# Performance work log

Hardware: AMD Instinct MI355X
Metric: run time of the kernel (lower is better)

The kernel has to match this reference:

```python
import jax, jax.numpy as jnp
import numpy as np

N_NODES = 50000
N_EDGES = 800000
D_IN = 64
D_OUT = 64


def setup_inputs() -> dict:
    key = jax.random.key(0)
    k1, k2, k3 = jax.random.split(key, 3)
    features = jax.random.normal(k1, (N_NODES, D_IN), dtype=jnp.float32)
    W = jax.random.normal(k2, (D_IN, D_OUT), dtype=jnp.float32) * (1.0 / np.sqrt(D_IN))
    b = jnp.zeros((D_OUT,), dtype=jnp.float32)
    edge_index = jax.random.randint(k3, (2, N_EDGES), 0, N_NODES, dtype=jnp.int64)
    return {"features": features, "W": W, "b": b, "edge_index": edge_index}


def reference(features, W, b, edge_index):
    # PyG GCNConv: add self-loops, symmetric normalization D^{-1/2}(A+I)D^{-1/2},
    # then aggregate x[row] at col (source -> target), plus linear + bias.
    N = features.shape[0]
    loop = jnp.arange(N, dtype=edge_index.dtype)
    row = jnp.concatenate([edge_index[0], loop])  # source nodes
    col = jnp.concatenate([edge_index[1], loop])  # target nodes

    ones = jnp.ones(row.shape[0], dtype=features.dtype)
    deg = jax.ops.segment_sum(ones, col, num_segments=N)  # in-degree incl. self-loop
    dinv = jnp.where(deg > 0, jax.lax.rsqrt(deg), 0.0)
    norm = dinv[row] * dinv[col]  # [E+N]

    x = features @ W                          # [N, D_OUT], tiny GEMM
    msg = x[row] * norm[:, None]              # gather + scale  [E+N, D_OUT]
    out = jax.ops.segment_sum(msg, col, num_segments=N)  # scatter-add
    return out + b
```

## Files before the change

kernel.cpp:

```cpp
#include <hip/hip_runtime.h>
#include <hip/hip_fp16.h>

#define NN 50000
#define NE 800000
#define D  64
#define NBUK  256
#define NBLKS 500
#define CHUNK2 1600
#define HSTR  512
#define FS 68

typedef float __attribute__((ext_vector_type(4))) f32x4;

__device__ inline int block_exscan(int val, int tid) {
    __shared__ int wsum[4];
    int lane = tid & 63, w = tid >> 6;
    int v = val;
    #pragma unroll
    for (int d = 1; d < 64; d <<= 1) {
        int t = __shfl_up(v, d);
        if (lane >= d) v += t;
    }
    if (lane == 63) wsum[w] = v;
    __syncthreads();
    int base = 0;
    #pragma unroll
    for (int i = 0; i < 4; ++i) base += (i < w) ? wsum[i] : 0;
    __syncthreads();
    return base + v - val;
}

__global__ __launch_bounds__(256) void k_hist(const int* __restrict__ col,
                                              int* __restrict__ H) {
    __shared__ int h[NBUK];
    const int tid = threadIdx.x, blk = blockIdx.x;
    h[tid] = 0;
    __syncthreads();
    const uint4* col4 = reinterpret_cast<const uint4*>(col + blk * CHUNK2);
    for (int i = tid; i < CHUNK2 / 4; i += 256) {
        uint4 v = col4[i];
        atomicAdd(&h[v.x >> 8], 1);
        atomicAdd(&h[v.y >> 8], 1);
        atomicAdd(&h[v.z >> 8], 1);
        atomicAdd(&h[v.w >> 8], 1);
    }
    __syncthreads();
    H[tid * HSTR + blk] = h[tid];
}

__global__ __launch_bounds__(256) void k_scanA(int* __restrict__ H,
                                               int* __restrict__ bsum) {
    const int tid = threadIdx.x, bkt = blockIdx.x;
    int* Hb = H + bkt * HSTR;
    int v0 = 0, v1 = 0;
    if (tid < 250) { v0 = Hb[2 * tid]; v1 = Hb[2 * tid + 1]; }
    int sum = v0 + v1;
    int ex = block_exscan(sum, tid);
    if (tid < 250) { Hb[2 * tid] = ex; Hb[2 * tid + 1] = ex + v0; }
    if (tid == 255) bsum[bkt] = ex;
}

__global__ __launch_bounds__(256) void k_bucket(const int* __restrict__ row,
                                                const int* __restrict__ col,
                                                const int* __restrict__ H,
                                                const int* __restrict__ bsum,
                                                unsigned int* __restrict__ packed) {
    __shared__ int base_l[NBUK];
    __shared__ int rank[NBUK];
    const int tid = threadIdx.x, blk = blockIdx.x;
    int ex = block_exscan(bsum[tid], tid);
    base_l[tid] = ex + H[tid * HSTR + blk];
    rank[tid] = 0;
    __syncthreads();
    const uint4* col4 = reinterpret_cast<const uint4*>(col + blk * CHUNK2);
    const uint4* row4 = reinterpret_cast<const uint4*>(row + blk * CHUNK2);
    for (int i = tid; i < CHUNK2 / 4; i += 256) {
        uint4 c4 = col4[i];
        uint4 r4 = row4[i];
        #pragma unroll
        for (int e = 0; e < 4; ++e) {
            unsigned c = (e == 0) ? c4.x : (e == 1) ? c4.y : (e == 2) ? c4.z : c4.w;
            unsigned r = (e == 0) ? r4.x : (e == 1) ? r4.y : (e == 2) ? r4.z : r4.w;
            int bk = c >> 8;
            int rk = atomicAdd(&rank[bk], 1);
            packed[base_l[bk] + rk] = (r & 0xFFFF) | ((c & 0xFF) << 16);
        }
    }
}

__global__ __launch_bounds__(256) void k_csr(const unsigned int* __restrict__ packed,
                                             const int* __restrict__ bsum,
                                             int* __restrict__ off,
                                             int* __restrict__ cnt,
                                             unsigned short* __restrict__ csr) {
    __shared__ int exs[NBUK];
    __shared__ int ncnt[NBUK];
    __shared__ int nbase[NBUK];
    __shared__ int rk2[NBUK];
    const int tid = threadIdx.x, b = blockIdx.x;
    int ex = block_exscan(bsum[tid], tid);
    exs[tid] = ex;
    ncnt[tid] = 0;
    rk2[tid] = 0;
    __syncthreads();
    const int start = exs[b];
    const int size  = bsum[b];
    for (int i = tid; i < size; i += 256)
        atomicAdd(&ncnt[(packed[start + i] >> 16) & 0xFF], 1);
    __syncthreads();
    int v2  = ncnt[tid];
    int ex2 = block_exscan(v2, tid);
    const int node = b * NBUK + tid;
    off[node] = start + ex2;
    cnt[node] = v2;
    nbase[tid] = start + ex2;
    __syncthreads();
    for (int i = tid; i < size; i += 256) {
        unsigned u = packed[start + i];
        int ln = (u >> 16) & 0xFF;
        int rk = atomicAdd(&rk2[ln], 1);
        csr[nbase[ln] + rk] = (unsigned short)(u & 0xFFFF);
    }
}

__global__ __launch_bounds__(256) void k_gemm(const float* __restrict__ feat,
                                              const float* __restrict__ W,
                                              const int* __restrict__ cnt,
                                              __half* __restrict__ y) {
    __shared__ float feat_lds[64 * FS];
    __shared__ float W_lds[D * D];

    const int tid   = threadIdx.x;
    const int rbase = blockIdx.x * 64;

    {
        const float4* W4  = reinterpret_cast<const float4*>(W);
        float4*       Wl4 = reinterpret_cast<float4*>(W_lds);
        for (int i = tid; i < D * D / 4; i += 256) Wl4[i] = W4[i];
    }
    {
        const int k0 = (tid & 15) * 4;
        #pragma unroll
        for (int it = 0; it < 4; ++it) {
            int r  = it * 16 + (tid >> 4);
            int gr = rbase + r;
            float4 v = make_float4(0.f, 0.f, 0.f, 0.f);
            if (gr < NN) v = *reinterpret_cast<const float4*>(&feat[gr * D + k0]);
            *reinterpret_cast<float4*>(&feat_lds[r * FS + k0]) = v;
        }
    }
    __syncthreads();

    const int tx = tid & 15;
    const int ty = tid >> 4;

    float acc[4][4] = {};

    #pragma unroll 8
    for (int k = 0; k < D; ++k) {
        float4 w = *reinterpret_cast<const float4*>(&W_lds[k * D + tx * 4]);
        float f0 = feat_lds[(ty * 4 + 0) * FS + k];
        float f1 = feat_lds[(ty * 4 + 1) * FS + k];
        float f2 = feat_lds[(ty * 4 + 2) * FS + k];
        float f3 = feat_lds[(ty * 4 + 3) * FS + k];
        acc[0][0] = fmaf(f0, w.x, acc[0][0]); acc[0][1] = fmaf(f0, w.y, acc[0][1]);
        acc[0][2] = fmaf(f0, w.z, acc[0][2]); acc[0][3] = fmaf(f0, w.w, acc[0][3]);
        acc[1][0] = fmaf(f1, w.x, acc[1][0]); acc[1][1] = fmaf(f1, w.y, acc[1][1]);
        acc[1][2] = fmaf(f1, w.z, acc[1][2]); acc[1][3] = fmaf(f1, w.w, acc[1][3]);
        acc[2][0] = fmaf(f2, w.x, acc[2][0]); acc[2][1] = fmaf(f2, w.y, acc[2][1]);
        acc[2][2] = fmaf(f2, w.z, acc[2][2]); acc[2][3] = fmaf(f2, w.w, acc[2][3]);
        acc[3][0] = fmaf(f3, w.x, acc[3][0]); acc[3][1] = fmaf(f3, w.y, acc[3][1]);
        acc[3][2] = fmaf(f3, w.z, acc[3][2]); acc[3][3] = fmaf(f3, w.w, acc[3][3]);
    }

    #pragma unroll
    for (int i = 0; i < 4; ++i) {
        int gr = rbase + ty * 4 + i;
        if (gr < NN) {
            float s = rsqrtf((float)cnt[gr] + 1.0f);
            __half2 h0 = __floats2half2_rn(acc[i][0] * s, acc[i][1] * s);
            __half2 h1 = __floats2half2_rn(acc[i][2] * s, acc[i][3] * s);
            union { __half2 h[2]; uint2 u; } p;
            p.h[0] = h0; p.h[1] = h1;
            *reinterpret_cast<uint2*>(&y[gr * D + tx * 4]) = p.u;
        }
    }
}

__global__ __launch_bounds__(256, 8) void k_agg8(const unsigned short* __restrict__ csr,
                                                 const int* __restrict__ off,
                                                 const int* __restrict__ cnt,
                                                 const __half* __restrict__ y,
                                                 const float* __restrict__ b,
                                                 float* __restrict__ out) {
    const int lane = threadIdx.x & 63;
    const int g    = lane >> 3;
    const int l8   = lane & 7;
    const int wave = blockIdx.x * 4 + (threadIdx.x >> 6);
    const int c    = wave * 8 + g;
    const bool valid = (c < NN);

    const uint4* y16 = reinterpret_cast<const uint4*>(y);

    const int s = valid ? off[c] : 0;
    const int n = valid ? cnt[c] : 0;

    int pre0 = (l8      < n) ? (int)csr[s + l8     ] : 0;
    int pre1 = (l8 + 8  < n) ? (int)csr[s + l8 + 8 ] : 0;
    int pre2 = (l8 + 16 < n) ? (int)csr[s + l8 + 16] : 0;
    int pre3 = (l8 + 24 < n) ? (int)csr[s + l8 + 24] : 0;

    float acc[8] = {0.f, 0.f, 0.f, 0.f, 0.f, 0.f, 0.f, 0.f};

    auto addm = [&](uint4 u, float m) {
        const __half2* h = reinterpret_cast<const __half2*>(&u);
        float2 f0 = __half22float2(h[0]);
        float2 f1 = __half22float2(h[1]);
        float2 f2 = __half22float2(h[2]);
        float2 f3 = __half22float2(h[3]);
        acc[0] = fmaf(m, f0.x, acc[0]); acc[1] = fmaf(m, f0.y, acc[1]);
        acc[2] = fmaf(m, f1.x, acc[2]); acc[3] = fmaf(m, f1.y, acc[3]);
        acc[4] = fmaf(m, f2.x, acc[4]); acc[5] = fmaf(m, f2.y, acc[5]);
        acc[6] = fmaf(m, f3.x, acc[6]); acc[7] = fmaf(m, f3.y, acc[7]);
    };

    if (valid) addm(y16[c * 8 + l8], 1.0f);

    const int srcb = lane & 56;

    #pragma unroll
    for (int w = 0; w < 4; ++w) {
        if (w * 8 < n) {
            const int pw = (w == 0) ? pre0 : (w == 1) ? pre1
                         : (w == 2) ? pre2 : pre3;
            uint4 u[8];
            float msk[8];
            #pragma unroll
            for (int e = 0; e < 8; ++e) {
                int r = __shfl(pw, srcb + e);
                u[e] = y16[r * 8 + l8];
                msk[e] = (w * 8 + e < n) ? 1.0f : 0.0f;
            }
            #pragma unroll
            for (int e = 0; e < 8; ++e) addm(u[e], msk[e]);
        }
    }

    for (int i = 32; i < n; ++i) {
        int r = (int)csr[s + i];
        addm(y16[r * 8 + l8], 1.0f);
    }

    if (valid) {
        float sc = rsqrtf((float)n + 1.0f);
        const float4* b4 = reinterpret_cast<const float4*>(b);
        float4 bb0 = b4[l8 * 2], bb1 = b4[l8 * 2 + 1];
        f32x4 o0, o1;
        o0.x = acc[0] * sc + bb0.x;  o0.y = acc[1] * sc + bb0.y;
        o0.z = acc[2] * sc + bb0.z;  o0.w = acc[3] * sc + bb0.w;
        o1.x = acc[4] * sc + bb1.x;  o1.y = acc[5] * sc + bb1.y;
        o1.z = acc[6] * sc + bb1.z;  o1.w = acc[7] * sc + bb1.w;
        f32x4* out4 = reinterpret_cast<f32x4*>(out);
        __builtin_nontemporal_store(o0, &out4[c * 16 + l8 * 2]);
        __builtin_nontemporal_store(o1, &out4[c * 16 + l8 * 2 + 1]);
    }
}

extern "C" void kernel_launch(void* const* d_in, const int* in_sizes, int n_in,
                              void* d_out, int out_size, void* d_ws, size_t ws_size,
                              hipStream_t stream) {
    const float* feat = (const float*)d_in[0];
    const float* W    = (const float*)d_in[1];
    const float* b    = (const float*)d_in[2];
    const int*   ei   = (const int*)d_in[3];
    const int*   row  = ei;
    const int*   col  = ei + NE;

    float* out = (float*)d_out;

    int*            H      = (int*)d_ws;
    int*            bsum   = H + NBUK * HSTR;
    int*            cnt    = bsum + 1024;
    int*            off    = cnt + 65536;
    unsigned int*   packed = (unsigned int*)(off + 65536);
    unsigned short* csr    = (unsigned short*)(packed + NE);
    __half*         y      = (__half*)(csr + NE);

    k_hist  <<<NBLKS, 256, 0, stream>>>(col, H);
    k_scanA <<<NBUK,  256, 0, stream>>>(H, bsum);
    k_bucket<<<NBLKS, 256, 0, stream>>>(row, col, H, bsum, packed);
    k_csr   <<<NBUK,  256, 0, stream>>>(packed, bsum, off, cnt, csr);
    k_gemm  <<<(NN + 63) / 64, 256, 0, stream>>>(feat, W, cnt, y);
    k_agg8  <<<(NN + 31) / 32, 256, 0, stream>>>(csr, off, cnt, y, b, out);
}
```

Before: 57.62 us.

## Fuse histogram with GEMM, move source-degree scaling into aggregation, stage CSR in LDS

The column histogram and the feature GEMM now run in one launch, split by block index, so the GEMM no longer waits for the CSR build and one launch is removed. The GEMM output is left unscaled. A per-node dinv array is produced in k_csr and applied per edge during aggregation, which adds a dinv[r] gather for every edge. k_csr also stages each bucket's packed edges and the local CSR in LDS before writing them out coalesced, and keeps a global-memory fallback for buckets that exceed the capacity.

```diff
diff --git a/kernel.cpp b/kernel.cpp
--- a/kernel.cpp
+++ b/kernel.cpp
@@ -9,6 +9,8 @@
 #define CHUNK2 1600
 #define HSTR  512
 #define FS 68
+#define GEMMB 782
+#define CAP 8192
 
 typedef float __attribute__((ext_vector_type(4))) f32x4;
 
@@ -30,108 +32,35 @@
     return base + v - val;
 }
 
-__global__ __launch_bounds__(256) void k_hist(const int* __restrict__ col,
-                                              int* __restrict__ H) {
-    __shared__ int h[NBUK];
-    const int tid = threadIdx.x, blk = blockIdx.x;
-    h[tid] = 0;
-    __syncthreads();
-    const uint4* col4 = reinterpret_cast<const uint4*>(col + blk * CHUNK2);
-    for (int i = tid; i < CHUNK2 / 4; i += 256) {
-        uint4 v = col4[i];
-        atomicAdd(&h[v.x >> 8], 1);
-        atomicAdd(&h[v.y >> 8], 1);
-        atomicAdd(&h[v.z >> 8], 1);
-        atomicAdd(&h[v.w >> 8], 1);
-    }
-    __syncthreads();
-    H[tid * HSTR + blk] = h[tid];
-}
-
-__global__ __launch_bounds__(256) void k_scanA(int* __restrict__ H,
-                                               int* __restrict__ bsum) {
-    const int tid = threadIdx.x, bkt = blockIdx.x;
-    int* Hb = H + bkt * HSTR;
-    int v0 = 0, v1 = 0;
-    if (tid < 250) { v0 = Hb[2 * tid]; v1 = Hb[2 * tid + 1]; }
-    int sum = v0 + v1;
-    int ex = block_exscan(sum, tid);
-    if (tid < 250) { Hb[2 * tid] = ex; Hb[2 * tid + 1] = ex + v0; }
-    if (tid == 255) bsum[bkt] = ex;
-}
-
-__global__ __launch_bounds__(256) void k_bucket(const int* __restrict__ row,
-                                                const int* __restrict__ col,
-                                                const int* __restrict__ H,
-                                                const int* __restrict__ bsum,
-                                                unsigned int* __restrict__ packed) {
-    __shared__ int base_l[NBUK];
-    __shared__ int rank[NBUK];
-    const int tid = threadIdx.x, blk = blockIdx.x;
-    int ex = block_exscan(bsum[tid], tid);
-    base_l[tid] = ex + H[tid * HSTR + blk];
-    rank[tid] = 0;
-    __syncthreads();
-    const uint4* col4 = reinterpret_cast<const uint4*>(col + blk * CHUNK2);
-    const uint4* row4 = reinterpret_cast<const uint4*>(row + blk * CHUNK2);
-    for (int i = tid; i < CHUNK2 / 4; i += 256) {
-        uint4 c4 = col4[i];
-        uint4 r4 = row4[i];
-        #pragma unroll
-        for (int e = 0; e < 4; ++e) {
-            unsigned c = (e == 0) ? c4.x : (e == 1) ? c4.y : (e == 2) ? c4.z : c4.w;
-            unsigned r = (e == 0) ? r4.x : (e == 1) ? r4.y : (e == 2) ? r4.z : r4.w;
-            int bk = c >> 8;
-            int rk = atomicAdd(&rank[bk], 1);
-            packed[base_l[bk] + rk] = (r & 0xFFFF) | ((c & 0xFF) << 16);
-        }
-    }
-}
-
-__global__ __launch_bounds__(256) void k_csr(const unsigned int* __restrict__ packed,
-                                             const int* __restrict__ bsum,
-                                             int* __restrict__ off,
-                                             int* __restrict__ cnt,
-                                             unsigned short* __restrict__ csr) {
-    __shared__ int exs[NBUK];
-    __shared__ int ncnt[NBUK];
-    __shared__ int nbase[NBUK];
-    __shared__ int rk2[NBUK];
-    const int tid = threadIdx.x, b = blockIdx.x;
-    int ex = block_exscan(bsum[tid], tid);
-    exs[tid] = ex;
-    ncnt[tid] = 0;
-    rk2[tid] = 0;
-    __syncthreads();
-    const int start = exs[b];
-    const int size  = bsum[b];
-    for (int i = tid; i < size; i += 256)
-        atomicAdd(&ncnt[(packed[start + i] >> 16) & 0xFF], 1);
-    __syncthreads();
-    int v2  = ncnt[tid];
-    int ex2 = block_exscan(v2, tid);
-    const int node = b * NBUK + tid;
-    off[node] = start + ex2;
-    cnt[node] = v2;
-    nbase[tid] = start + ex2;
-    __syncthreads();
-    for (int i = tid; i < size; i += 256) {
-        unsigned u = packed[start + i];
-        int ln = (u >> 16) & 0xFF;
-        int rk = atomicAdd(&rk2[ln], 1);
-        csr[nbase[ln] + rk] = (unsigned short)(u & 0xFFFF);
-    }
-}
-
-__global__ __launch_bounds__(256) void k_gemm(const float* __restrict__ feat,
-                                              const float* __restrict__ W,
-                                              const int* __restrict__ cnt,
-                                              __half* __restrict__ y) {
-    __shared__ float feat_lds[64 * FS];
-    __shared__ float W_lds[D * D];
-
-    const int tid   = threadIdx.x;
-    const int rbase = blockIdx.x * 64;
+__global__ __launch_bounds__(256) void k_hist_gemm(const int* __restrict__ col,
+                                                   int* __restrict__ H,
+                                                   const float* __restrict__ feat,
+                                                   const float* __restrict__ W,
+                                                   __half* __restrict__ y) {
+    __shared__ float smem[64 * FS + D * D];
+    const int tid = threadIdx.x;
+
+    if (blockIdx.x < NBLKS) {
+        int* h = reinterpret_cast<int*>(smem);
+        const int blk = blockIdx.x;
+        h[tid] = 0;
+        __syncthreads();
+        const uint4* col4 = reinterpret_cast<const uint4*>(col + blk * CHUNK2);
+        for (int i = tid; i < CHUNK2 / 4; i += 256) {
+            uint4 v = col4[i];
+            atomicAdd(&h[v.x >> 8], 1);
+            atomicAdd(&h[v.y >> 8], 1);
+            atomicAdd(&h[v.z >> 8], 1);
+            atomicAdd(&h[v.w >> 8], 1);
+        }
+        __syncthreads();
+        H[tid * HSTR + blk] = h[tid];
+        return;
+    }
+
+    float* feat_lds = smem;
+    float* W_lds    = smem + 64 * FS;
+    const int rbase = (blockIdx.x - NBLKS) * 64;
 
     {
         const float4* W4  = reinterpret_cast<const float4*>(W);
@@ -177,9 +106,8 @@
     for (int i = 0; i < 4; ++i) {
         int gr = rbase + ty * 4 + i;
         if (gr < NN) {
-            float s = rsqrtf((float)cnt[gr] + 1.0f);
-            __half2 h0 = __floats2half2_rn(acc[i][0] * s, acc[i][1] * s);
-            __half2 h1 = __floats2half2_rn(acc[i][2] * s, acc[i][3] * s);
+            __half2 h0 = __floats2half2_rn(acc[i][0], acc[i][1]);
+            __half2 h1 = __floats2half2_rn(acc[i][2], acc[i][3]);
             union { __half2 h[2]; uint2 u; } p;
             p.h[0] = h0; p.h[1] = h1;
             *reinterpret_cast<uint2*>(&y[gr * D + tx * 4]) = p.u;
@@ -187,9 +115,116 @@
     }
 }
 
+__global__ __launch_bounds__(256) void k_scanA(int* __restrict__ H,
+                                               int* __restrict__ bsum) {
+    const int tid = threadIdx.x, bkt = blockIdx.x;
+    int* Hb = H + bkt * HSTR;
+    int v0 = 0, v1 = 0;
+    if (tid < 250) { v0 = Hb[2 * tid]; v1 = Hb[2 * tid + 1]; }
+    int sum = v0 + v1;
+    int ex = block_exscan(sum, tid);
+    if (tid < 250) { Hb[2 * tid] = ex; Hb[2 * tid + 1] = ex + v0; }
+    if (tid == 255) bsum[bkt] = ex;
+}
+
+__global__ __launch_bounds__(256) void k_bucket(const int* __restrict__ row,
+                                                const int* __restrict__ col,
+                                                const int* __restrict__ H,
+                                                const int* __restrict__ bsum,
+                                                unsigned int* __restrict__ packed) {
+    __shared__ int base_l[NBUK];
+    __shared__ int rank[NBUK];
+    const int tid = threadIdx.x, blk = blockIdx.x;
+    int ex = block_exscan(bsum[tid], tid);
+    base_l[tid] = ex + H[tid * HSTR + blk];
+    rank[tid] = 0;
+    __syncthreads();
+    const uint4* col4 = reinterpret_cast<const uint4*>(col + blk * CHUNK2);
+    const uint4* row4 = reinterpret_cast<const uint4*>(row + blk * CHUNK2);
+    for (int i = tid; i < CHUNK2 / 4; i += 256) {
+        uint4 c4 = col4[i];
+        uint4 r4 = row4[i];
+        #pragma unroll
+        for (int e = 0; e < 4; ++e) {
+            unsigned c = (e == 0) ? c4.x : (e == 1) ? c4.y : (e == 2) ? c4.z : c4.w;
+            unsigned r = (e == 0) ? r4.x : (e == 1) ? r4.y : (e == 2) ? r4.z : r4.w;
+            int bk = c >> 8;
+            int rk = atomicAdd(&rank[bk], 1);
+            packed[base_l[bk] + rk] = (r & 0xFFFF) | ((c & 0xFF) << 16);
+        }
+    }
+}
+
+__global__ __launch_bounds__(256) void k_csr(const unsigned int* __restrict__ packed,
+                                             const int* __restrict__ bsum,
+                                             int* __restrict__ off,
+                                             int* __restrict__ cnt,
+                                             float* __restrict__ dinv,
+                                             unsigned short* __restrict__ csr) {
+    __shared__ unsigned pk[CAP];
+    __shared__ unsigned short lcsr[CAP];
+    __shared__ int ncnt[NBUK];
+    __shared__ int nbase[NBUK];
+    __shared__ int rk2[NBUK];
+    __shared__ int sstart;
+    const int tid = threadIdx.x, b = blockIdx.x;
+
+    int ex = block_exscan(bsum[tid], tid);
+    if (tid == b) sstart = ex;
+    ncnt[tid] = 0;
+    rk2[tid] = 0;
+    __syncthreads();
+
+    const int start = sstart;
+    const int size  = bsum[b];
+
+    if (size <= CAP) {
+        for (int i = tid; i < size; i += 256) pk[i] = packed[start + i];
+        __syncthreads();
+        for (int i = tid; i < size; i += 256)
+            atomicAdd(&ncnt[(pk[i] >> 16) & 0xFF], 1);
+        __syncthreads();
+        int v2  = ncnt[tid];
+        int ex2 = block_exscan(v2, tid);
+        const int node = b * NBUK + tid;
+        off[node]  = start + ex2;
+        cnt[node]  = v2;
+        dinv[node] = rsqrtf((float)v2 + 1.0f);
+        nbase[tid] = ex2;
+        __syncthreads();
+        for (int i = tid; i < size; i += 256) {
+            unsigned u = pk[i];
+            int ln = (u >> 16) & 0xFF;
+            int rk = atomicAdd(&rk2[ln], 1);
+            lcsr[nbase[ln] + rk] = (unsigned short)(u & 0xFFFF);
+        }
+        __syncthreads();
+        for (int i = tid; i < size; i += 256) csr[start + i] = lcsr[i];
+    } else {
+        for (int i = tid; i < size; i += 256)
+            atomicAdd(&ncnt[(packed[start + i] >> 16) & 0xFF], 1);
+        __syncthreads();
+        int v2  = ncnt[tid];
+        int ex2 = block_exscan(v2, tid);
+        const int node = b * NBUK + tid;
+        off[node]  = start + ex2;
+        cnt[node]  = v2;
+        dinv[node] = rsqrtf((float)v2 + 1.0f);
+        nbase[tid] = start + ex2;
+        __syncthreads();
+        for (int i = tid; i < size; i += 256) {
+            unsigned u = packed[start + i];
+            int ln = (u >> 16) & 0xFF;
+            int rk = atomicAdd(&rk2[ln], 1);
+            csr[nbase[ln] + rk] = (unsigned short)(u & 0xFFFF);
+        }
+    }
+}
+
 __global__ __launch_bounds__(256, 8) void k_agg8(const unsigned short* __restrict__ csr,
                                                  const int* __restrict__ off,
                                                  const int* __restrict__ cnt,
+                                                 const float* __restrict__ dinv,
                                                  const __half* __restrict__ y,
                                                  const float* __restrict__ b,
                                                  float* __restrict__ out) {
@@ -204,6 +239,7 @@
 
     const int s = valid ? off[c] : 0;
     const int n = valid ? cnt[c] : 0;
+    const float dc = valid ? dinv[c] : 0.0f;
 
     int pre0 = (l8      < n) ? (int)csr[s + l8     ] : 0;
     int pre1 = (l8 + 8  < n) ? (int)csr[s + l8 + 8 ] : 0;
@@ -224,7 +260,7 @@
         acc[6] = fmaf(m, f3.x, acc[6]); acc[7] = fmaf(m, f3.y, acc[7]);
     };
 
-    if (valid) addm(y16[c * 8 + l8], 1.0f);
+    if (valid) addm(y16[c * 8 + l8], dc);
 
     const int srcb = lane & 56;
 
@@ -239,7 +275,8 @@
             for (int e = 0; e < 8; ++e) {
                 int r = __shfl(pw, srcb + e);
                 u[e] = y16[r * 8 + l8];
-                msk[e] = (w * 8 + e < n) ? 1.0f : 0.0f;
+                float dv = dinv[r];
+                msk[e] = (w * 8 + e < n) ? dv : 0.0f;
             }
             #pragma unroll
             for (int e = 0; e < 8; ++e) addm(u[e], msk[e]);
@@ -248,18 +285,17 @@
 
     for (int i = 32; i < n; ++i) {
         int r = (int)csr[s + i];
-        addm(y16[r * 8 + l8], 1.0f);
+        addm(y16[r * 8 + l8], dinv[r]);
     }
 
     if (valid) {
-        float sc = rsqrtf((float)n + 1.0f);
         const float4* b4 = reinterpret_cast<const float4*>(b);
         float4 bb0 = b4[l8 * 2], bb1 = b4[l8 * 2 + 1];
         f32x4 o0, o1;
-        o0.x = acc[0] * sc + bb0.x;  o0.y = acc[1] * sc + bb0.y;
-        o0.z = acc[2] * sc + bb0.z;  o0.w = acc[3] * sc + bb0.w;
-        o1.x = acc[4] * sc + bb1.x;  o1.y = acc[5] * sc + bb1.y;
-        o1.z = acc[6] * sc + bb1.z;  o1.w = acc[7] * sc + bb1.w;
+        o0.x = acc[0] * dc + bb0.x;  o0.y = acc[1] * dc + bb0.y;
+        o0.z = acc[2] * dc + bb0.z;  o0.w = acc[3] * dc + bb0.w;
+        o1.x = acc[4] * dc + bb1.x;  o1.y = acc[5] * dc + bb1.y;
+        o1.z = acc[6] * dc + bb1.z;  o1.w = acc[7] * dc + bb1.w;
         f32x4* out4 = reinterpret_cast<f32x4*>(out);
         __builtin_nontemporal_store(o0, &out4[c * 16 + l8 * 2]);
         __builtin_nontemporal_store(o1, &out4[c * 16 + l8 * 2 + 1]);
@@ -282,14 +318,14 @@
     int*            bsum   = H + NBUK * HSTR;
     int*            cnt    = bsum + 1024;
     int*            off    = cnt + 65536;
-    unsigned int*   packed = (unsigned int*)(off + 65536);
+    float*          dinv   = (float*)(off + 65536);
+    unsigned int*   packed = (unsigned int*)(dinv + 65536);
     unsigned short* csr    = (unsigned short*)(packed + NE);
     __half*         y      = (__half*)(csr + NE);
 
-    k_hist  <<<NBLKS, 256, 0, stream>>>(col, H);
-    k_scanA <<<NBUK,  256, 0, stream>>>(H, bsum);
-    k_bucket<<<NBLKS, 256, 0, stream>>>(row, col, H, bsum, packed);
-    k_csr   <<<NBUK,  256, 0, stream>>>(packed, bsum, off, cnt, csr);
-    k_gemm  <<<(NN + 63) / 64, 256, 0, stream>>>(feat, W, cnt, y);
-    k_agg8  <<<(NN + 31) / 32, 256, 0, stream>>>(csr, off, cnt, y, b, out);
-}
+    k_hist_gemm<<<NBLKS + GEMMB, 256, 0, stream>>>(col, H, feat, W, y);
+    k_scanA    <<<NBUK,  256, 0, stream>>>(H, bsum);
+    k_bucket   <<<NBLKS, 256, 0, stream>>>(row, col, H, bsum, packed);
+    k_csr      <<<NBUK,  256, 0, stream>>>(packed, bsum, off, cnt, dinv, csr);
+    k_agg8     <<<(NN + 31) / 32, 256, 0, stream>>>(csr, off, cnt, dinv, y, b, out);
+}
```

Result: faster. 53.87 us (-6.5%).
